# Kernel tuning notes

Measured on AMD Instinct MI355X. Metric: run time of the kernel, lower is better.

The kernel has to match this reference:

```python
import jax, jax.numpy as jnp
import numpy as np

def setup_inputs() -> dict:
    key = jax.random.key(0)
    k1, k2 = jax.random.split(key)
    B, T, D = 32, 8192, 512
    x = jax.random.normal(k1, (B, T, D), dtype=jnp.float32)
    w = jax.random.normal(k2, (D, 1), dtype=jnp.float32) * (1.0 / np.sqrt(D))
    b = jnp.zeros((1,), dtype=jnp.float32)
    return {"x": x, "w": w, "b": b}

def reference(x, w, b):
    # scores: [B, T] = Linear(d_m -> 1) squeezed
    scores = jnp.einsum('btd,d->bt', x, w[:, 0]) + b[0]
    # softmax over seq dim (dim=2 after transpose in original == T here)
    attn = jax.nn.softmax(scores, axis=-1)  # [B, T]
    # weighted sum: [B, 1, D]
    out = jnp.einsum('bt,btd->bd', attn, x)[:, None, :]
    return out
```

## Files before the change

kernel.cpp:

```cpp
#include <hip/hip_runtime.h>
#include <math.h>

#define D_MODEL 512

typedef float fx4 __attribute__((ext_vector_type(4)));

#define NTL(p) __builtin_nontemporal_load((const fx4*)(p))

__device__ __forceinline__ float dot8(const fx4& a0, const fx4& a1,
                                      const fx4& b0, const fx4& b1) {
    return a0.x * b0.x + a0.y * b0.y + a0.z * b0.z + a0.w * b0.w
         + a1.x * b1.x + a1.y * b1.y + a1.z * b1.z + a1.w * b1.w;
}

__device__ __forceinline__ void process4(
    const fx4& r0a, const fx4& r0b, const fx4& r1a, const fx4& r1b,
    const fx4& r2a, const fx4& r2b, const fx4& r3a, const fx4& r3b,
    const fx4& wa, const fx4& wb,
    float& m, float& l, fx4& a0, fx4& a1)
{
    float d0 = dot8(r0a, r0b, wa, wb);
    float d1 = dot8(r1a, r1b, wa, wb);
    float d2 = dot8(r2a, r2b, wa, wb);
    float d3 = dot8(r3a, r3b, wa, wb);
    #pragma unroll
    for (int off = 32; off >= 1; off >>= 1) {
        d0 += __shfl_xor(d0, off);
        d1 += __shfl_xor(d1, off);
        d2 += __shfl_xor(d2, off);
        d3 += __shfl_xor(d3, off);
    }
    const float mx = fmaxf(fmaxf(d0, d1), fmaxf(d2, d3));
    if (mx > m) {
        const float sc = __expf(m - mx);
        l *= sc;
        a0 *= sc;
        a1 *= sc;
        m = mx;
    }
    const float p0 = __expf(d0 - m);
    const float p1 = __expf(d1 - m);
    const float p2 = __expf(d2 - m);
    const float p3 = __expf(d3 - m);
    l += (p0 + p1) + (p2 + p3);
    a0 += p0 * r0a; a1 += p0 * r0b;
    a0 += p1 * r1a; a1 += p1 * r1b;
    a0 += p2 * r2a; a1 += p2 * r2b;
    a0 += p3 * r3a; a1 += p3 * r3b;
}

__global__ __launch_bounds__(256) void pool_pass1(
    const float* __restrict__ x, const float* __restrict__ w,
    float* __restrict__ acc_ws, float* __restrict__ ml_ws,
    int T, int C, int RPW)
{
    const int b    = blockIdx.y;
    const int wave = threadIdx.x >> 6;
    const int lane = threadIdx.x & 63;
    const int chunk = blockIdx.x * 4 + wave;

    const fx4 wa = *(const fx4*)(w + 4 * lane);
    const fx4 wb = *(const fx4*)(w + 256 + 4 * lane);

    float m = -INFINITY, l = 0.0f;
    fx4 a0 = (fx4)0.0f;
    fx4 a1 = (fx4)0.0f;

    const float* xr = x + (size_t)b * T * D_MODEL + (size_t)chunk * RPW * D_MODEL;

    fx4 c0a = NTL(xr                   + 4 * lane);
    fx4 c0b = NTL(xr             + 256 + 4 * lane);
    fx4 c1a = NTL(xr + 1*D_MODEL       + 4 * lane);
    fx4 c1b = NTL(xr + 1*D_MODEL + 256 + 4 * lane);
    fx4 c2a = NTL(xr + 2*D_MODEL       + 4 * lane);
    fx4 c2b = NTL(xr + 2*D_MODEL + 256 + 4 * lane);
    fx4 c3a = NTL(xr + 3*D_MODEL       + 4 * lane);
    fx4 c3b = NTL(xr + 3*D_MODEL + 256 + 4 * lane);

    for (int r = 0; r < RPW - 4; r += 4) {
        xr += 4 * D_MODEL;
        const fx4 n0a = NTL(xr                   + 4 * lane);
        const fx4 n0b = NTL(xr             + 256 + 4 * lane);
        const fx4 n1a = NTL(xr + 1*D_MODEL       + 4 * lane);
        const fx4 n1b = NTL(xr + 1*D_MODEL + 256 + 4 * lane);
        const fx4 n2a = NTL(xr + 2*D_MODEL       + 4 * lane);
        const fx4 n2b = NTL(xr + 2*D_MODEL + 256 + 4 * lane);
        const fx4 n3a = NTL(xr + 3*D_MODEL       + 4 * lane);
        const fx4 n3b = NTL(xr + 3*D_MODEL + 256 + 4 * lane);

        process4(c0a, c0b, c1a, c1b, c2a, c2b, c3a, c3b, wa, wb, m, l, a0, a1);

        c0a = n0a; c0b = n0b; c1a = n1a; c1b = n1b;
        c2a = n2a; c2b = n2b; c3a = n3a; c3b = n3b;
    }
    process4(c0a, c0b, c1a, c1b, c2a, c2b, c3a, c3b, wa, wb, m, l, a0, a1);

    float* accp = acc_ws + (size_t)(b * C + chunk) * D_MODEL;
    *(fx4*)(accp + 4 * lane)       = a0;
    *(fx4*)(accp + 256 + 4 * lane) = a1;
    if (lane == 0) {
        ml_ws[(b * C + chunk) * 2 + 0] = m;
        ml_ws[(b * C + chunk) * 2 + 1] = l;
    }
}

__global__ __launch_bounds__(256) void pool_pass2(
    const float* __restrict__ acc_ws, const float* __restrict__ ml_ws,
    float* __restrict__ out, int C)
{
    const int b   = blockIdx.x;
    const int q   = blockIdx.y;
    const int tid = threadIdx.x;
    const int fx  = tid & 31;
    const int cg  = tid >> 5;

    __shared__ float s_e[256];
    __shared__ float red[256];
    __shared__ fx4   s_acc[256];

    float mloc = -INFINITY;
    for (int c = tid; c < C; c += 256)
        mloc = fmaxf(mloc, ml_ws[(b * C + c) * 2 + 0]);
    red[tid] = mloc;
    __syncthreads();
    for (int s = 128; s > 0; s >>= 1) {
        if (tid < s) red[tid] = fmaxf(red[tid], red[tid + s]);
        __syncthreads();
    }
    const float M = red[0];
    __syncthreads();

    float lloc = 0.0f;
    for (int c = tid; c < C; c += 256) {
        const float e = __expf(ml_ws[(b * C + c) * 2 + 0] - M);
        s_e[c] = e;
        lloc += e * ml_ws[(b * C + c) * 2 + 1];
    }
    red[tid] = lloc;
    __syncthreads();
    for (int s = 128; s > 0; s >>= 1) {
        if (tid < s) red[tid] += red[tid + s];
        __syncthreads();
    }
    const float L = red[0];
    __syncthreads();

    fx4 sum = (fx4)0.0f;
    const float* base = acc_ws + (size_t)b * C * D_MODEL + q * 128 + fx * 4;
    for (int c = cg; c < C; c += 8) {
        sum += s_e[c] * *(const fx4*)(base + (size_t)c * D_MODEL);
    }
    s_acc[tid] = sum;
    __syncthreads();
    if (cg == 0) {
        fx4 t = s_acc[fx];
        #pragma unroll
        for (int g = 1; g < 8; ++g) t += s_acc[g * 32 + fx];
        const float inv = 1.0f / L;
        t *= inv;
        float* op = out + b * D_MODEL + q * 128 + fx * 4;
        *(fx4*)op = t;
    }
}

extern "C" void kernel_launch(void* const* d_in, const int* in_sizes, int n_in,
                              void* d_out, int out_size, void* d_ws, size_t ws_size,
                              hipStream_t stream)
{
    const float* x = (const float*)d_in[0];
    const float* w = (const float*)d_in[1];
    float* out = (float*)d_out;

    const int D = D_MODEL;
    const int B = 32;
    const int T = in_sizes[0] / (B * D);

    int C = 128;
    while (C > 8) {
        size_t need = (size_t)B * C * D * sizeof(float) + (size_t)B * C * 2 * sizeof(float);
        if (need <= ws_size) break;
        C >>= 1;
    }
    const int RPW = T / C;

    float* acc_ws = (float*)d_ws;
    float* ml_ws  = acc_ws + (size_t)B * C * D;

    dim3 grid1(C / 4, B);
    pool_pass1<<<grid1, 256, 0, stream>>>(x, w, acc_ws, ml_ws, T, C, RPW);
    pool_pass2<<<dim3(B, 4), 256, 0, stream>>>(acc_ws, ml_ws, out, C);
}
```

Before: 101.9 us.

## Fuse split-softmax merge into pass1 via last-block atomic counter

Merges the two kernels into one: each block writes its partial (m, l, acc) results, then bumps a per-batch atomic counter, and the last block to finish for a batch does the cross-chunk softmax merge and writes the output. This removes the second kernel launch and its dependency gap, and it adds a memset of the counters before the launch. The trade-off is that the final reduction for each batch now runs on a single 256-thread block instead of four, serially over all C chunks.

```diff
diff --git a/kernel.cpp b/kernel.cpp
--- a/kernel.cpp
+++ b/kernel.cpp
@@ -49,74 +49,74 @@
     a0 += p3 * r3a; a1 += p3 * r3b;
 }
 
-__global__ __launch_bounds__(256) void pool_pass1(
+__global__ __launch_bounds__(256) void pool_fused(
     const float* __restrict__ x, const float* __restrict__ w,
     float* __restrict__ acc_ws, float* __restrict__ ml_ws,
+    unsigned int* __restrict__ cnt, float* __restrict__ out,
     int T, int C, int RPW)
 {
     const int b    = blockIdx.y;
     const int wave = threadIdx.x >> 6;
     const int lane = threadIdx.x & 63;
     const int chunk = blockIdx.x * 4 + wave;
+    const int tid  = threadIdx.x;
 
-    const fx4 wa = *(const fx4*)(w + 4 * lane);
-    const fx4 wb = *(const fx4*)(w + 256 + 4 * lane);
+    __shared__ unsigned int s_old;
+    __shared__ float s_e[256];
+    __shared__ float red[256];
 
-    float m = -INFINITY, l = 0.0f;
-    fx4 a0 = (fx4)0.0f;
-    fx4 a1 = (fx4)0.0f;
+    {
+        const fx4 wa = *(const fx4*)(w + 4 * lane);
+        const fx4 wb = *(const fx4*)(w + 256 + 4 * lane);
 
-    const float* xr = x + (size_t)b * T * D_MODEL + (size_t)chunk * RPW * D_MODEL;
+        float m = -INFINITY, l = 0.0f;
+        fx4 a0 = (fx4)0.0f;
+        fx4 a1 = (fx4)0.0f;
 
-    fx4 c0a = NTL(xr                   + 4 * lane);
-    fx4 c0b = NTL(xr             + 256 + 4 * lane);
-    fx4 c1a = NTL(xr + 1*D_MODEL       + 4 * lane);
-    fx4 c1b = NTL(xr + 1*D_MODEL + 256 + 4 * lane);
-    fx4 c2a = NTL(xr + 2*D_MODEL       + 4 * lane);
-    fx4 c2b = NTL(xr + 2*D_MODEL + 256 + 4 * lane);
-    fx4 c3a = NTL(xr + 3*D_MODEL       + 4 * lane);
-    fx4 c3b = NTL(xr + 3*D_MODEL + 256 + 4 * lane);
+        const float* xr = x + (size_t)b * T * D_MODEL + (size_t)chunk * RPW * D_MODEL;
 
-    for (int r = 0; r < RPW - 4; r += 4) {
-        xr += 4 * D_MODEL;
-        const fx4 n0a = NTL(xr                   + 4 * lane);
-        const fx4 n0b = NTL(xr             + 256 + 4 * lane);
-        const fx4 n1a = NTL(xr + 1*D_MODEL       + 4 * lane);
-        const fx4 n1b = NTL(xr + 1*D_MODEL + 256 + 4 * lane);
-        const fx4 n2a = NTL(xr + 2*D_MODEL       + 4 * lane);
-        const fx4 n2b = NTL(xr + 2*D_MODEL + 256 + 4 * lane);
-        const fx4 n3a = NTL(xr + 3*D_MODEL       + 4 * lane);
-        const fx4 n3b = NTL(xr + 3*D_MODEL + 256 + 4 * lane);
+        fx4 c0a = NTL(xr                   + 4 * lane);
+        fx4 c0b = NTL(xr             + 256 + 4 * lane);
+        fx4 c1a = NTL(xr + 1*D_MODEL       + 4 * lane);
+        fx4 c1b = NTL(xr + 1*D_MODEL + 256 + 4 * lane);
+        fx4 c2a = NTL(xr + 2*D_MODEL       + 4 * lane);
+        fx4 c2b = NTL(xr + 2*D_MODEL + 256 + 4 * lane);
+        fx4 c3a = NTL(xr + 3*D_MODEL       + 4 * lane);
+        fx4 c3b = NTL(xr + 3*D_MODEL + 256 + 4 * lane);
 
+        for (int r = 0; r < RPW - 4; r += 4) {
+            xr += 4 * D_MODEL;
+            const fx4 n0a = NTL(xr                   + 4 * lane);
+            const fx4 n0b = NTL(xr             + 256 + 4 * lane);
+            const fx4 n1a = NTL(xr + 1*D_MODEL       + 4 * lane);
+            const fx4 n1b = NTL(xr + 1*D_MODEL + 256 + 4 * lane);
+            const fx4 n2a = NTL(xr + 2*D_MODEL       + 4 * lane);
+            const fx4 n2b = NTL(xr + 2*D_MODEL + 256 + 4 * lane);
+            const fx4 n3a = NTL(xr + 3*D_MODEL       + 4 * lane);
+            const fx4 n3b = NTL(xr + 3*D_MODEL + 256 + 4 * lane);
+
+            process4(c0a, c0b, c1a, c1b, c2a, c2b, c3a, c3b, wa, wb, m, l, a0, a1);
+
+            c0a = n0a; c0b = n0b; c1a = n1a; c1b = n1b;
+            c2a = n2a; c2b = n2b; c3a = n3a; c3b = n3b;
+        }
         process4(c0a, c0b, c1a, c1b, c2a, c2b, c3a, c3b, wa, wb, m, l, a0, a1);
 
-        c0a = n0a; c0b = n0b; c1a = n1a; c1b = n1b;
-        c2a = n2a; c2b = n2b; c3a = n3a; c3b = n3b;
+        float* accp = acc_ws + (size_t)(b * C + chunk) * D_MODEL;
+        *(fx4*)(accp + 4 * lane)       = a0;
+        *(fx4*)(accp + 256 + 4 * lane) = a1;
+        if (lane == 0) {
+            ml_ws[(b * C + chunk) * 2 + 0] = m;
+            ml_ws[(b * C + chunk) * 2 + 1] = l;
+        }
     }
-    process4(c0a, c0b, c1a, c1b, c2a, c2b, c3a, c3b, wa, wb, m, l, a0, a1);
 
-    float* accp = acc_ws + (size_t)(b * C + chunk) * D_MODEL;
-    *(fx4*)(accp + 4 * lane)       = a0;
-    *(fx4*)(accp + 256 + 4 * lane) = a1;
-    if (lane == 0) {
-        ml_ws[(b * C + chunk) * 2 + 0] = m;
-        ml_ws[(b * C + chunk) * 2 + 1] = l;
-    }
-}
-
-__global__ __launch_bounds__(256) void pool_pass2(
-    const float* __restrict__ acc_ws, const float* __restrict__ ml_ws,
-    float* __restrict__ out, int C)
-{
-    const int b   = blockIdx.x;
-    const int q   = blockIdx.y;
-    const int tid = threadIdx.x;
-    const int fx  = tid & 31;
-    const int cg  = tid >> 5;
-
-    __shared__ float s_e[256];
-    __shared__ float red[256];
-    __shared__ fx4   s_acc[256];
+    __threadfence();
+    __syncthreads();
+    if (tid == 0) s_old = atomicAdd(&cnt[b], 1u);
+    __syncthreads();
+    if (s_old != (unsigned)(C / 4 - 1)) return;
+    __threadfence();
 
     float mloc = -INFINITY;
     for (int c = tid; c < C; c += 256)
@@ -143,24 +143,17 @@
         __syncthreads();
     }
     const float L = red[0];
-    __syncthreads();
 
-    fx4 sum = (fx4)0.0f;
-    const float* base = acc_ws + (size_t)b * C * D_MODEL + q * 128 + fx * 4;
-    for (int c = cg; c < C; c += 8) {
-        sum += s_e[c] * *(const fx4*)(base + (size_t)c * D_MODEL);
+    float s0 = 0.0f, s1 = 0.0f;
+    const float* basep = acc_ws + (size_t)b * C * D_MODEL;
+    for (int c = 0; c < C; ++c) {
+        const float e = s_e[c];
+        s0 = fmaf(e, basep[(size_t)c * D_MODEL + tid], s0);
+        s1 = fmaf(e, basep[(size_t)c * D_MODEL + tid + 256], s1);
     }
-    s_acc[tid] = sum;
-    __syncthreads();
-    if (cg == 0) {
-        fx4 t = s_acc[fx];
-        #pragma unroll
-        for (int g = 1; g < 8; ++g) t += s_acc[g * 32 + fx];
-        const float inv = 1.0f / L;
-        t *= inv;
-        float* op = out + b * D_MODEL + q * 128 + fx * 4;
-        *(fx4*)op = t;
-    }
+    const float inv = 1.0f / L;
+    out[b * D_MODEL + tid]       = s0 * inv;
+    out[b * D_MODEL + tid + 256] = s1 * inv;
 }
 
 extern "C" void kernel_launch(void* const* d_in, const int* in_sizes, int n_in,
@@ -177,7 +170,9 @@
 
     int C = 128;
     while (C > 8) {
-        size_t need = (size_t)B * C * D * sizeof(float) + (size_t)B * C * 2 * sizeof(float);
+        size_t need = (size_t)B * C * D * sizeof(float)
+                    + (size_t)B * C * 2 * sizeof(float)
+                    + (size_t)B * sizeof(unsigned int);
         if (need <= ws_size) break;
         C >>= 1;
     }
@@ -185,8 +180,10 @@
 
     float* acc_ws = (float*)d_ws;
     float* ml_ws  = acc_ws + (size_t)B * C * D;
+    unsigned int* cnt = (unsigned int*)(ml_ws + (size_t)B * C * 2);
 
-    dim3 grid1(C / 4, B);
-    pool_pass1<<<grid1, 256, 0, stream>>>(x, w, acc_ws, ml_ws, T, C, RPW);
-    pool_pass2<<<dim3(B, 4), 256, 0, stream>>>(acc_ws, ml_ws, out, C);
+    hipMemsetAsync(cnt, 0, B * sizeof(unsigned int), stream);
+
+    dim3 grid(C / 4, B);
+    pool_fused<<<grid, 256, 0, stream>>>(x, w, acc_ws, ml_ws, cnt, out, T, C, RPW);
 }
```

After: 320.1 us. +214.3%, slower.
